# Optimization experiments

Measured on AMD Instinct MI355X. Metric: run time of the kernel, lower is better.

Reference implementation:

```python
import jax, jax.numpy as jnp
import numpy as np

B, OUT, IN = 2048, 4096, 4096
KEEPRATE = 0.5  # mid-training drop schedule state; first-call default masks nothing


def setup_inputs() -> dict:
    key = jax.random.key(0)
    k1, k2, k3, k4 = jax.random.split(key, 4)
    data = jax.random.normal(k1, (B, IN), dtype=jnp.float32)
    # weight parameter = fftn of a real N(0, 0.1) matrix, stored as complex
    w0 = jax.random.normal(k2, (OUT, IN), dtype=jnp.float32) * 0.1
    wc = jnp.fft.fftn(w0.astype(jnp.float32))
    w_real = jnp.real(wc).astype(jnp.float32)
    w_imag = jnp.imag(wc).astype(jnp.float32)
    bias = jax.random.normal(k3, (OUT,), dtype=jnp.float32) * 0.1
    # ZMAT: rank assignment, a permutation of 0..OUT*IN-1
    zmat = jax.random.permutation(k4, jnp.arange(OUT * IN, dtype=jnp.int64)).reshape(OUT, IN)
    return {"data": data, "w_real": w_real, "w_imag": w_imag, "bias": bias, "zmat": zmat}


def reference(data, w_real, w_imag, bias, zmat):
    O, I = w_real.shape
    numel = O * I
    threval = KEEPRATE * numel
    # IDROP: keep entries whose rank <= threshold (ZMAT > threval -> 0)
    idrop = (zmat.astype(jnp.float32) <= threval).astype(w_real.dtype)
    dropweight = (w_real + 1j * w_imag) * idrop  # masked FFT-domain weight
    # torch.fft.irfftn(dropweight, s=(O, I)): full ifft on dim 0, real irfft on dim 1
    # (numpy/jax irfft crops the last axis to I//2+1, same as torch)
    w_spatial = jnp.fft.irfftn(dropweight, s=(O, I), axes=(0, 1)).astype(data.dtype)
    return data @ w_spatial.T + bias
```

## Files before the change

### kernel.cpp

```cpp
#include <hip/hip_runtime.h>
#include <hip/hip_bf16.h>
#include <stdint.h>

#define OUT_N 4096
#define IN_N  4096
#define BATCH 2048
#define KHALF 2049

typedef __bf16 bf16x8 __attribute__((ext_vector_type(8)));
typedef float  f32x4  __attribute__((ext_vector_type(4)));

__device__ __forceinline__ unsigned short f2bf(float f) {
  unsigned int u = __builtin_bit_cast(unsigned int, f);
  u += 0x7FFFu + ((u >> 16) & 1u);
  return (unsigned short)(u >> 16);
}

__device__ __forceinline__ float2 cmul(float2 a, float2 b) {
  return make_float2(a.x * b.x - a.y * b.y, a.x * b.y + a.y * b.x);
}
__device__ __forceinline__ float2 cadd(float2 a, float2 b) { return make_float2(a.x + b.x, a.y + b.y); }
__device__ __forceinline__ float2 csub(float2 a, float2 b) { return make_float2(a.x - b.x, a.y - b.y); }
__device__ __forceinline__ float2 muli(float2 a) { return make_float2(-a.y, a.x); }

__device__ __forceinline__ void dft4i(float2& x0, float2& x1, float2& x2, float2& x3) {
  float2 t0 = cadd(x0, x2), t1 = csub(x0, x2);
  float2 t2 = cadd(x1, x3), t3 = csub(x1, x3);
  float2 it3 = muli(t3);
  x0 = cadd(t0, t2); x2 = csub(t0, t2);
  x1 = cadd(t1, it3); x3 = csub(t1, it3);
}

#define C8f  0.70710678118654752f
#define C16f 0.92387953251128676f
#define S16f 0.38268343236508977f

__device__ __forceinline__ void dft16i(float2 r[16]) {
  float2 t[16];
#pragma unroll
  for (int b = 0; b < 4; ++b) {
    float2 a0 = r[b], a1 = r[4 + b], a2 = r[8 + b], a3 = r[12 + b];
    dft4i(a0, a1, a2, a3);
    t[b * 4 + 0] = a0; t[b * 4 + 1] = a1; t[b * 4 + 2] = a2; t[b * 4 + 3] = a3;
  }
  const float2 W1 = make_float2(C16f, S16f);
  const float2 W2 = make_float2(C8f, C8f);
  const float2 W3 = make_float2(S16f, C16f);
  const float2 W6 = make_float2(-C8f, C8f);
  const float2 W9 = make_float2(-C16f, -S16f);
  t[5]  = cmul(t[5],  W1);  t[6]  = cmul(t[6],  W2);  t[7]  = cmul(t[7],  W3);
  t[9]  = cmul(t[9],  W2);  t[10] = muli(t[10]);      t[11] = cmul(t[11], W6);
  t[13] = cmul(t[13], W3);  t[14] = cmul(t[14], W6);  t[15] = cmul(t[15], W9);
#pragma unroll
  for (int q = 0; q < 4; ++q) {
    float2 a0 = t[q], a1 = t[4 + q], a2 = t[8 + q], a3 = t[12 + q];
    dft4i(a0, a1, a2, a3);
    r[q] = a0; r[q + 4] = a1; r[q + 8] = a2; r[q + 12] = a3;
  }
}

__device__ __forceinline__ void twiddle16(float2 r[16], float theta) {
  float sn, cs;
  __sincosf(theta, &sn, &cs);
  float2 w = make_float2(cs, sn);
  float2 wk = w;
  r[1] = cmul(r[1], wk);
#pragma unroll
  for (int k = 2; k < 16; ++k) {
    wk = cmul(wk, w);
    r[k] = cmul(r[k], wk);
  }
}

__device__ void fft4096_core(float2 r[16], float2* lds, int t) {
  dft16i(r);
  twiddle16(r, 1.53398078788564123e-3f * (float)t);
#pragma unroll
  for (int k1 = 0; k1 < 16; ++k1) lds[k1 * 256 + (t ^ k1)] = r[k1];
  __syncthreads();
  const int k1 = t & 15, b = t >> 4;
  float2 s[16];
#pragma unroll
  for (int a = 0; a < 16; ++a) s[a] = lds[k1 * 256 + ((16 * a + b) ^ k1)];
  __syncthreads();
  dft16i(s);
  twiddle16(s, 2.45436926061702596e-2f * (float)b);
#pragma unroll
  for (int c = 0; c < 16; ++c) lds[k1 * 256 + ((c * 16 + b) ^ k1)] = s[c];
  __syncthreads();
#pragma unroll
  for (int bb = 0; bb < 16; ++bb) r[bb] = lds[k1 * 256 + ((b * 16 + bb) ^ k1)];
  dft16i(r);
}

__global__ void mask_transpose(const float* __restrict__ wr, const float* __restrict__ wi,
                               const int* __restrict__ zmat, float2* __restrict__ wt) {
  __shared__ float2 tile[32][65];
  const int tx = threadIdx.x;
  const int ty = threadIdx.y;
  const int o0 = blockIdx.y * 32;
  if (blockIdx.x == 32) {
    int t = ty * 32 + tx;
    if (t < 32) {
      int o = o0 + t;
      size_t idx = (size_t)o * IN_N + 2048;
      float2 v = make_float2(0.f, 0.f);
      if (zmat[idx] <= 8388608) v = make_float2(wr[idx], wi[idx]);
      wt[(size_t)2048 * OUT_N + o] = v;
    }
    return;
  }
  const int k0 = blockIdx.x * 64;
#pragma unroll
  for (int r = 0; r < 4; ++r) {
    int o = o0 + ty + r * 8;
    size_t base = (size_t)o * IN_N + k0 + tx * 2;
    float2 vr = *(const float2*)&wr[base];
    float2 vi = *(const float2*)&wi[base];
    int2   z  = *(const int2*)&zmat[base];
    tile[ty + r * 8][tx * 2]     = (z.x <= 8388608) ? make_float2(vr.x, vi.x) : make_float2(0.f, 0.f);
    tile[ty + r * 8][tx * 2 + 1] = (z.y <= 8388608) ? make_float2(vr.y, vi.y) : make_float2(0.f, 0.f);
  }
  __syncthreads();
#pragma unroll
  for (int rr = 0; rr < 8; ++rr) {
    int k = k0 + ty + rr * 8;
    int o = o0 + tx;
    wt[(size_t)k * OUT_N + o] = tile[tx][ty + rr * 8];
  }
}

__global__ __launch_bounds__(256) void col_ifft(float2* __restrict__ wt) {
  __shared__ float2 lds[4096];
  const int t = threadIdx.x;
  float2* row = wt + (size_t)blockIdx.x * OUT_N;
  float2 r[16];
#pragma unroll
  for (int n1 = 0; n1 < 16; ++n1) r[n1] = row[n1 * 256 + t];
  fft4096_core(r, lds, t);
#pragma unroll
  for (int d = 0; d < 16; ++d) row[t + 256 * d] = r[d];
}

__global__ void transpose_ko(const float2* __restrict__ yt, float2* __restrict__ y) {
  __shared__ float2 tile[32][33];
  const int k0 = blockIdx.x * 32;
  const int o0 = blockIdx.y * 32;
  const int tx = threadIdx.x;
  const int ty = threadIdx.y;
#pragma unroll
  for (int r = 0; r < 4; ++r) {
    int k = k0 + ty + r * 8;
    int o = o0 + tx;
    if (k < KHALF) tile[ty + r * 8][tx] = yt[(size_t)k * OUT_N + o];
  }
  __syncthreads();
#pragma unroll
  for (int r = 0; r < 4; ++r) {
    int o = o0 + ty + r * 8;
    int k = k0 + tx;
    if (k < KHALF) y[(size_t)o * KHALF + k] = tile[tx][ty + r * 8];
  }
}

__global__ __launch_bounds__(256) void row_irfft2(const float2* __restrict__ y,
                                                  unsigned short* __restrict__ wbf) {
  __shared__ float2 lds[4096];
  const int t = threadIdx.x;
  const int oa = blockIdx.x * 2, ob = oa + 1;
  const float2* rowa = y + (size_t)oa * KHALF;
  const float2* rowb = y + (size_t)ob * KHALF;
  float2* lsa = lds;
  float2* lsb = lds + 2048;
#pragma unroll
  for (int j = 0; j < 8; ++j) {
    int k = t + j * 256;
    lsa[k] = rowa[k]; lsb[k] = rowb[k];
  }
  __syncthreads();
  float2 r[16];
#pragma unroll
  for (int n1 = 0; n1 < 16; ++n1) {
    int m = n1 * 256 + t;
    float2 za, zb;
    if (m == 0)        { za = make_float2(lsa[0].x, 0.f);    zb = make_float2(lsb[0].x, 0.f); }
    else if (m < 2048) { za = lsa[m];                        zb = lsb[m]; }
    else if (m == 2048){ float2 na = rowa[2048], nb = rowb[2048];
                         za = make_float2(na.x, 0.f);        zb = make_float2(nb.x, 0.f); }
    else { float2 ua = lsa[4096 - m], ub = lsb[4096 - m];
           za = make_float2(ua.x, -ua.y); zb = make_float2(ub.x, -ub.y); }
    r[n1] = make_float2(za.x - zb.y, za.y + zb.x);
  }
  __syncthreads();
  fft4096_core(r, lds, t);
  const float sc = 1.0f / (4096.0f * 4096.0f);
  unsigned short* orow_a = wbf + (size_t)oa * IN_N;
  unsigned short* orow_b = wbf + (size_t)ob * IN_N;
#pragma unroll
  for (int d = 0; d < 16; ++d) {
    orow_a[t + 256 * d] = f2bf(r[d].x * sc);
    orow_b[t + 256 * d] = f2bf(r[d].y * sc);
  }
}

__global__ void cvt_bf16(const float* __restrict__ x, unsigned short* __restrict__ o, int n4) {
  int i = blockIdx.x * blockDim.x + threadIdx.x;
  if (i < n4) {
    float4 v = ((const float4*)x)[i];
    ushort4 r;
    r.x = f2bf(v.x); r.y = f2bf(v.y); r.z = f2bf(v.z); r.w = f2bf(v.w);
    ((ushort4*)o)[i] = r;
  }
}

#define BK 64
#define NT (IN_N / BK)

__device__ __forceinline__ void gload_lds16(const void* gp, void* lp) {
  typedef const __attribute__((address_space(1))) void* gptr_t;
  typedef __attribute__((address_space(3))) void* lptr_t;
  __builtin_amdgcn_global_load_lds((gptr_t)(unsigned long long)gp,
                                   (lptr_t)(unsigned int)(unsigned long long)lp,
                                   16, 0, 0);
}

__device__ __forceinline__ void stage_tile(const unsigned short* __restrict__ A,
                                           const unsigned short* __restrict__ B,
                                           unsigned short* as, unsigned short* bs,
                                           int gm0, int gn0, int kt,
                                           int r0, int srow, int schunk) {
#pragma unroll
  for (int j = 0; j < 4; ++j) {
    gload_lds16(A + ((size_t)(gm0 + r0 + j * 8 + srow) * IN_N + kt + schunk * 8),
                as + (size_t)(r0 + j * 8) * BK);
    gload_lds16(B + ((size_t)(gn0 + r0 + j * 8 + srow) * IN_N + kt + schunk * 8),
                bs + (size_t)(r0 + j * 8) * BK);
  }
}

__global__ __launch_bounds__(256) void gemm_bt_bias(const unsigned short* __restrict__ A,
                                                    const unsigned short* __restrict__ B,
                                                    const float* __restrict__ bias,
                                                    float* __restrict__ C) {
  __shared__ __align__(16) unsigned short As[2][128 * BK];
  __shared__ __align__(16) unsigned short Bs[2][128 * BK];
  const int tid  = threadIdx.x;
  const int wave = tid >> 6;
  const int lane = tid & 63;
  const int gm0 = blockIdx.y * 128;
  const int gn0 = blockIdx.x * 128;

  f32x4 acc[4][4] = {};
  const int wm = wave >> 1, wn = wave & 1;
  const int srow   = lane >> 3;
  const int schunk = (lane & 7) ^ srow;
  const int r0     = wave * 32;
  const int l7 = lane & 7;
  const int qbase = lane >> 4;
  const int fra = wm * 64 + (lane & 15);
  const int frb = wn * 64 + (lane & 15);

  stage_tile(A, B, As[0], Bs[0], gm0, gn0, 0,  r0, srow, schunk);
  stage_tile(A, B, As[1], Bs[1], gm0, gn0, BK, r0, srow, schunk);

  for (int t = 0; t < NT; ++t) {
    const int S = t & 1;
    if (t < NT - 1) asm volatile("s_waitcnt vmcnt(8)" ::: "memory");
    else            asm volatile("s_waitcnt vmcnt(0)" ::: "memory");
    __builtin_amdgcn_sched_barrier(0);
    __builtin_amdgcn_s_barrier();
    __builtin_amdgcn_sched_barrier(0);

#pragma unroll
    for (int kk = 0; kk < 2; ++kk) {
      bf16x8 af[4], bfr[4];
      const int q = kk * 4 + qbase;
#pragma unroll
      for (int i = 0; i < 4; ++i) {
        af[i]  = *(const bf16x8*)&As[S][(fra + i * 16) * BK + ((q ^ l7) * 8)];
        bfr[i] = *(const bf16x8*)&Bs[S][(frb + i * 16) * BK + ((q ^ l7) * 8)];
      }
#pragma unroll
      for (int mi = 0; mi < 4; ++mi)
#pragma unroll
        for (int ni = 0; ni < 4; ++ni)
          acc[mi][ni] = __builtin_amdgcn_mfma_f32_16x16x32_bf16(af[mi], bfr[ni], acc[mi][ni], 0, 0, 0);
    }
    __builtin_amdgcn_sched_barrier(0);
    __builtin_amdgcn_s_barrier();
    if (t + 2 < NT)
      stage_tile(A, B, As[S], Bs[S], gm0, gn0, (t + 2) * BK, r0, srow, schunk);
  }

  const int col0 = gn0 + wn * 64 + (lane & 15);
  const int row0 = gm0 + wm * 64 + (lane >> 4) * 4;
#pragma unroll
  for (int mi = 0; mi < 4; ++mi) {
#pragma unroll
    for (int ni = 0; ni < 4; ++ni) {
      int col = col0 + ni * 16;
      float bv = bias[col];
#pragma unroll
      for (int r = 0; r < 4; ++r) {
        int row = row0 + mi * 16 + r;
        C[(size_t)row * OUT_N + col] = acc[mi][ni][r] + bv;
      }
    }
  }
}

extern "C" void kernel_launch(void* const* d_in, const int* in_sizes, int n_in,
                              void* d_out, int out_size, void* d_ws, size_t ws_size,
                              hipStream_t stream) {
  const float* data = (const float*)d_in[0];
  const float* wr   = (const float*)d_in[1];
  const float* wi   = (const float*)d_in[2];
  const float* bias = (const float*)d_in[3];
  const int*   zmat = (const int*)d_in[4];

  char* ws = (char*)d_ws;
  float2* wt = (float2*)ws;
  float2* y  = (float2*)(ws + 67141632ull);
  unsigned short* wbf = (unsigned short*)ws;
  unsigned short* dbf = (unsigned short*)(ws + 33554432ull);

  hipLaunchKernelGGL(mask_transpose, dim3(33, 128), dim3(32, 8), 0, stream, wr, wi, zmat, wt);
  hipLaunchKernelGGL(col_ifft,       dim3(2049),    dim3(256),   0, stream, wt);
  hipLaunchKernelGGL(transpose_ko,   dim3(65, 128), dim3(32, 8), 0, stream, wt, y);
  hipLaunchKernelGGL(row_irfft2,     dim3(2048),    dim3(256),   0, stream, y, wbf);
  hipLaunchKernelGGL(cvt_bf16,       dim3(8192),    dim3(256),   0, stream, data, dbf, (BATCH * IN_N) / 4);
  hipLaunchKernelGGL(gemm_bt_bias,   dim3(OUT_N / 128, BATCH / 128), dim3(256), 0, stream,
                     dbf, wbf, bias, (float*)d_out);
}
```

Before: 354.5 us.

## Drop intermediate transpose; read column-FFT output directly in row irfft

Removes the transpose_ko kernel and its full intermediate buffer. row_irfft2 now gathers two adjacent output rows at once as float4 loads straight from the k-major column-FFT result, with a swizzled block index so that concurrently running blocks touch nearby addresses. This avoids one full read/write pass over about 64 MB of complex data and one kernel launch. In exchange, the loads are strided by 32 KB per k, and the workspace layout moves wbf and dbf to new offsets.

```diff
diff --git a/kernel.cpp b/kernel.cpp
--- a/kernel.cpp
+++ b/kernel.cpp
@@ -142,40 +142,19 @@
   for (int d = 0; d < 16; ++d) row[t + 256 * d] = r[d];
 }
 
-__global__ void transpose_ko(const float2* __restrict__ yt, float2* __restrict__ y) {
-  __shared__ float2 tile[32][33];
-  const int k0 = blockIdx.x * 32;
-  const int o0 = blockIdx.y * 32;
-  const int tx = threadIdx.x;
-  const int ty = threadIdx.y;
-#pragma unroll
-  for (int r = 0; r < 4; ++r) {
-    int k = k0 + ty + r * 8;
-    int o = o0 + tx;
-    if (k < KHALF) tile[ty + r * 8][tx] = yt[(size_t)k * OUT_N + o];
-  }
-  __syncthreads();
-#pragma unroll
-  for (int r = 0; r < 4; ++r) {
-    int o = o0 + ty + r * 8;
-    int k = k0 + tx;
-    if (k < KHALF) y[(size_t)o * KHALF + k] = tile[tx][ty + r * 8];
-  }
-}
-
-__global__ __launch_bounds__(256) void row_irfft2(const float2* __restrict__ y,
+__global__ __launch_bounds__(256) void row_irfft2(const float2* __restrict__ wt,
                                                   unsigned short* __restrict__ wbf) {
-  __shared__ float2 lds[4096];
+  __shared__ float4 lsf[2048];
   const int t = threadIdx.x;
-  const int oa = blockIdx.x * 2, ob = oa + 1;
-  const float2* rowa = y + (size_t)oa * KHALF;
-  const float2* rowb = y + (size_t)ob * KHALF;
-  float2* lsa = lds;
-  float2* lsb = lds + 2048;
+  const int bid = (int)blockIdx.x;
+  const int lb  = (bid & 7) * 256 + (bid >> 3);
+  const int oa = lb * 2, ob = oa + 1;
+  const float4* wt4 = (const float4*)wt;
+  const int oq = oa >> 1;
 #pragma unroll
   for (int j = 0; j < 8; ++j) {
     int k = t + j * 256;
-    lsa[k] = rowa[k]; lsb[k] = rowb[k];
+    lsf[k] = wt4[(size_t)k * 2048 + oq];
   }
   __syncthreads();
   float2 r[16];
@@ -183,16 +162,16 @@
   for (int n1 = 0; n1 < 16; ++n1) {
     int m = n1 * 256 + t;
     float2 za, zb;
-    if (m == 0)        { za = make_float2(lsa[0].x, 0.f);    zb = make_float2(lsb[0].x, 0.f); }
-    else if (m < 2048) { za = lsa[m];                        zb = lsb[m]; }
-    else if (m == 2048){ float2 na = rowa[2048], nb = rowb[2048];
-                         za = make_float2(na.x, 0.f);        zb = make_float2(nb.x, 0.f); }
-    else { float2 ua = lsa[4096 - m], ub = lsb[4096 - m];
-           za = make_float2(ua.x, -ua.y); zb = make_float2(ub.x, -ub.y); }
+    if (m == 0)        { float4 v = lsf[0];    za = make_float2(v.x, 0.f); zb = make_float2(v.z, 0.f); }
+    else if (m < 2048) { float4 v = lsf[m];    za = make_float2(v.x, v.y); zb = make_float2(v.z, v.w); }
+    else if (m == 2048){ float4 v = wt4[(size_t)2048 * 2048 + oq];
+                         za = make_float2(v.x, 0.f); zb = make_float2(v.z, 0.f); }
+    else { float4 v = lsf[4096 - m];
+           za = make_float2(v.x, -v.y); zb = make_float2(v.z, -v.w); }
     r[n1] = make_float2(za.x - zb.y, za.y + zb.x);
   }
   __syncthreads();
-  fft4096_core(r, lds, t);
+  fft4096_core(r, (float2*)lsf, t);
   const float sc = 1.0f / (4096.0f * 4096.0f);
   unsigned short* orow_a = wbf + (size_t)oa * IN_N;
   unsigned short* orow_b = wbf + (size_t)ob * IN_N;
@@ -320,14 +299,12 @@
 
   char* ws = (char*)d_ws;
   float2* wt = (float2*)ws;
-  float2* y  = (float2*)(ws + 67141632ull);
-  unsigned short* wbf = (unsigned short*)ws;
-  unsigned short* dbf = (unsigned short*)(ws + 33554432ull);
+  unsigned short* wbf = (unsigned short*)(ws + 67141632ull);
+  unsigned short* dbf = (unsigned short*)(ws + 100696064ull);
 
   hipLaunchKernelGGL(mask_transpose, dim3(33, 128), dim3(32, 8), 0, stream, wr, wi, zmat, wt);
   hipLaunchKernelGGL(col_ifft,       dim3(2049),    dim3(256),   0, stream, wt);
-  hipLaunchKernelGGL(transpose_ko,   dim3(65, 128), dim3(32, 8), 0, stream, wt, y);
-  hipLaunchKernelGGL(row_irfft2,     dim3(2048),    dim3(256),   0, stream, y, wbf);
+  hipLaunchKernelGGL(row_irfft2,     dim3(2048),    dim3(256),   0, stream, wt, wbf);
   hipLaunchKernelGGL(cvt_bf16,       dim3(8192),    dim3(256),   0, stream, data, dbf, (BATCH * IN_N) / 4);
   hipLaunchKernelGGL(gemm_bt_bias,   dim3(OUT_N / 128, BATCH / 128), dim3(256), 0, stream,
                      dbf, wbf, bias, (float*)d_out);
```

Result: faster. 328.7 us (-7.3%).
